# Optimization experiments

Hardware: AMD Instinct MI355X
Metric: run time of the kernel (lower is better)

## Reference

```python
import jax, jax.numpy as jnp
import numpy as np

FLOW_NUM = 2048
H = 64  # lstm_output_dim
NOISE_DIM = 3


def _w(key, shape, s=0.08):
    return (jax.random.normal(key, shape, dtype=jnp.float32) * s)


def setup_inputs() -> dict:
    key = jax.random.key(0)
    ks = jax.random.split(key, 20)
    d = {
        "noise": jax.random.normal(ks[0], (FLOW_NUM, NOISE_DIM), dtype=jnp.float32),
        "w_ih0": _w(ks[1], (4 * H, NOISE_DIM)),
        "w_hh0": _w(ks[2], (4 * H, H)),
        "b_ih0": _w(ks[3], (4 * H,)),
        "b_hh0": _w(ks[4], (4 * H,)),
        "w_ih1": _w(ks[5], (4 * H, H)),
        "w_hh1": _w(ks[6], (4 * H, H)),
        "b_ih1": _w(ks[7], (4 * H,)),
        "b_hh1": _w(ks[8], (4 * H,)),
        "w_ih2": _w(ks[9], (4 * H, H)),
        "w_hh2": _w(ks[10], (4 * H, H)),
        "b_ih2": _w(ks[11], (4 * H,)),
        "b_hh2": _w(ks[12], (4 * H,)),
        "fc1_w": _w(ks[13], (32, H)),
        "fc1_b": _w(ks[14], (32,)),
        "fc2_w": _w(ks[15], (16, 32)),
        "fc2_b": _w(ks[16], (16,)),
        "fc3_w": _w(ks[17], (3, 16)),
        "fc3_b": _w(ks[18], (3,)),
        "flow_length": 500,
    }
    return d


def _lstm_cell(x, h, c, w_ih, w_hh, b_ih, b_hh):
    # PyTorch gate order: input, forget, cell(g), output
    gates = x @ w_ih.T + h @ w_hh.T + (b_ih + b_hh)
    i, f, g, o = jnp.split(gates, 4, axis=-1)
    c_new = jax.nn.sigmoid(f) * c + jax.nn.sigmoid(i) * jnp.tanh(g)
    h_new = jax.nn.sigmoid(o) * jnp.tanh(c_new)
    return h_new, c_new


def reference(noise, w_ih0, w_hh0, b_ih0, b_hh0,
              w_ih1, w_hh1, b_ih1, b_hh1,
              w_ih2, w_hh2, b_ih2, b_hh2,
              fc1_w, fc1_b, fc2_w, fc2_b, fc3_w, fc3_b,
              flow_length):
    layers = [(w_ih0, w_hh0, b_ih0, b_hh0),
              (w_ih1, w_hh1, b_ih1, b_hh1),
              (w_ih2, w_hh2, b_ih2, b_hh2)]
    n = noise.shape[0]
    h0 = jnp.zeros((3, n, H), dtype=noise.dtype)
    c0 = jnp.zeros((3, n, H), dtype=noise.dtype)

    def step(carry, _):
        x, h, c = carry
        inp = x
        hs, cs = [], []
        for l, (wi, wh, bi, bh) in enumerate(layers):
            h_l, c_l = _lstm_cell(inp, h[l], c[l], wi, wh, bi, bh)
            hs.append(h_l)
            cs.append(c_l)
            inp = h_l
        # MLP head (Dropout is identity in eval mode); LeakyReLU slope 0.01
        y = jax.nn.leaky_relu(inp @ fc1_w.T + fc1_b)
        y = jax.nn.leaky_relu(y @ fc2_w.T + fc2_b)
        y = jax.nn.leaky_relu(y @ fc3_w.T + fc3_b)
        return (y, jnp.stack(hs), jnp.stack(cs)), y

    _, flow = jax.lax.scan(step, (noise, h0, c0), None, length=flow_length)
    # flow: [flow_length, flow_num, 3] -> [flow_num, flow_length, 3]
    return jnp.swapaxes(flow, 0, 1)
```

## Files before the change

### kernel.cpp

```cpp
#include <hip/hip_runtime.h>

#define NT 512

typedef _Float16 f16x8 __attribute__((ext_vector_type(8)));
typedef _Float16 f16x4 __attribute__((ext_vector_type(4)));
typedef float    f32x4 __attribute__((ext_vector_type(4)));

#define MFMA(a, b, c) __builtin_amdgcn_mfma_f32_16x16x32_f16((a), (b), (c), 0, 0, 0)

#if __has_builtin(__builtin_amdgcn_exp2f)
__device__ __forceinline__ float fexp(float x) { return __builtin_amdgcn_exp2f(x * 1.4426950408889634f); }
#else
__device__ __forceinline__ float fexp(float x) { return __expf(x); }
#endif
#if __has_builtin(__builtin_amdgcn_rcpf)
__device__ __forceinline__ float frcp(float x) { return __builtin_amdgcn_rcpf(x); }
#else
__device__ __forceinline__ float frcp(float x) { return 1.0f / x; }
#endif
__device__ __forceinline__ float sigm(float x)  { return frcp(1.0f + fexp(-x)); }
__device__ __forceinline__ float tanh_(float x) { return 1.0f - 2.0f * frcp(1.0f + fexp(2.0f * x)); }
__device__ __forceinline__ float lrelu(float x) { return x > 0.0f ? x : 0.01f * x; }

__device__ __forceinline__ f16x8 ld8(const float* p) {
    const float4* q = (const float4*)p;
    float4 a = q[0], b = q[1];
    f16x8 r = { (_Float16)a.x, (_Float16)a.y, (_Float16)a.z, (_Float16)a.w,
                (_Float16)b.x, (_Float16)b.y, (_Float16)b.z, (_Float16)b.w };
    return r;
}

__global__ __launch_bounds__(NT, 2)
void gen_kernel(
    const float* __restrict__ noise,
    const float* __restrict__ w_ih0, const float* __restrict__ w_hh0,
    const float* __restrict__ b_ih0, const float* __restrict__ b_hh0,
    const float* __restrict__ w_ih1, const float* __restrict__ w_hh1,
    const float* __restrict__ b_ih1, const float* __restrict__ b_hh1,
    const float* __restrict__ w_ih2, const float* __restrict__ w_hh2,
    const float* __restrict__ b_ih2, const float* __restrict__ b_hh2,
    const float* __restrict__ fc1_w, const float* __restrict__ fc1_b,
    const float* __restrict__ fc2_w, const float* __restrict__ fc2_b,
    const float* __restrict__ fc3_w, const float* __restrict__ fc3_b,
    const int*   __restrict__ flow_len_p,
    float* __restrict__ out)
{
    __shared__ _Float16 sh[3][2][16 * 64] __attribute__((aligned(16)));
    __shared__ _Float16 sx [16][40] __attribute__((aligned(16)));
    __shared__ _Float16 sy1[16][40] __attribute__((aligned(16)));
    __shared__ _Float16 sy2[16][40] __attribute__((aligned(16)));

    const int tid  = threadIdx.x;
    const int l    = tid & 63;
    const int w    = tid >> 6;
    const int ls   = l & 15;
    const int lj   = l >> 4;
    const int base = blockIdx.x * 8;
    const int T    = flow_len_p[0];

    const int gA  = ls & 3;
    const int rA0 = gA * 64 + 4 * (2 * w + 0) + (ls >> 2);
    const int rA1 = gA * 64 + 4 * (2 * w + 1) + (ls >> 2);

    f16x8 A1[2][4], A2[2][4], A0[2][3];
#pragma unroll
    for (int kc = 0; kc < 2; ++kc) {
        A1[0][kc]     = ld8(w_ih1 + rA0 * 64 + 32 * kc + 8 * lj);
        A1[1][kc]     = ld8(w_ih1 + rA1 * 64 + 32 * kc + 8 * lj);
        A1[0][2 + kc] = ld8(w_hh1 + rA0 * 64 + 32 * kc + 8 * lj);
        A1[1][2 + kc] = ld8(w_hh1 + rA1 * 64 + 32 * kc + 8 * lj);
        A2[0][kc]     = ld8(w_ih2 + rA0 * 64 + 32 * kc + 8 * lj);
        A2[1][kc]     = ld8(w_ih2 + rA1 * 64 + 32 * kc + 8 * lj);
        A2[0][2 + kc] = ld8(w_hh2 + rA0 * 64 + 32 * kc + 8 * lj);
        A2[1][2 + kc] = ld8(w_hh2 + rA1 * 64 + 32 * kc + 8 * lj);
        A0[0][kc]     = ld8(w_hh0 + rA0 * 64 + 32 * kc + 8 * lj);
        A0[1][kc]     = ld8(w_hh0 + rA1 * 64 + 32 * kc + 8 * lj);
    }
#pragma unroll
    for (int tt = 0; tt < 2; ++tt) {
        const int r = tt ? rA1 : rA0;
        f16x8 v;
#pragma unroll
        for (int i = 0; i < 8; ++i) {
            int kl = 8 * lj + i;
            float x = (kl < 3) ? w_ih0[r * 3 + kl]
                    : (kl == 3) ? (b_ih0[r] + b_hh0[r]) : 0.0f;
            v[i] = (_Float16)x;
        }
        A0[tt][2] = v;
    }
    f16x8 F1[2][2], F2, F3;
#pragma unroll
    for (int tt = 0; tt < 2; ++tt)
#pragma unroll
        for (int kc = 0; kc < 2; ++kc)
            F1[tt][kc] = ld8(fc1_w + (16 * tt + ls) * 64 + 32 * kc + 8 * lj);
    F2 = ld8(fc2_w + ls * 32 + 8 * lj);
    {
        f16x8 v;
#pragma unroll
        for (int i = 0; i < 8; ++i) {
            int k = 8 * lj + i;
            v[i] = (_Float16)((ls < 3 && k < 16) ? fc3_w[ls * 16 + k] : 0.0f);
        }
        F3 = v;
    }
    const int uc0 = 8 * w + lj, uc1 = 8 * w + 4 + lj;
    const int u_own = (ls < 8) ? uc0 : uc1;
    const int cs    = ls & 7;
    const int whaddr = cs * 64 + 8 * (((u_own >> 3) + cs) & 7) + (u_own & 7);
    float b1o[4], b2o[4];
#pragma unroll
    for (int g = 0; g < 4; ++g) {
        b1o[g] = b_ih1[g * 64 + u_own] + b_hh1[g * 64 + u_own];
        b2o[g] = b_ih2[g * 64 + u_own] + b_hh2[g * 64 + u_own];
    }
    float hb1a[4], hb1b[4], hb2[4];
#pragma unroll
    for (int r = 0; r < 4; ++r) {
        hb1a[r] = fc1_b[4 * lj + r];
        hb1b[r] = fc1_b[16 + 4 * lj + r];
        hb2[r]  = fc2_b[4 * lj + r];
    }
    float fb3[3] = { fc3_b[0], fc3_b[1], fc3_b[2] };

    for (int i = tid; i < 3 * 2 * 16 * 64; i += NT) ((_Float16*)sh)[i] = (_Float16)0.0f;
    for (int i = tid; i < 16 * 40; i += NT) {
        ((_Float16*)sx)[i]  = (_Float16)0.0f;
        ((_Float16*)sy1)[i] = (_Float16)0.0f;
        ((_Float16*)sy2)[i] = (_Float16)0.0f;
    }
    __syncthreads();
    if (tid < 16) sx[tid][3] = (_Float16)1.0f;
    if (tid < 24) {
        int s = tid / 3, d = tid % 3;
        sx[s][d] = (_Float16)noise[(base + s) * 3 + d];
    }

    float c0s = 0.0f, c1s = 0.0f, c2s = 0.0f;
    const float zb[4] = {0, 0, 0, 0};
    __syncthreads();

#define RD(L, p, kg) (*(const f16x8*)&sh[L][p][ls * 64 + 8 * (((kg) + ls) & 7)])

#define REPACK(cell, a0, a1)                                                   \
    float cell[4];                                                             \
    _Pragma("unroll")                                                          \
    for (int r = 0; r < 4; ++r) {                                              \
        float v_ = __shfl_xor(a1[r], 8);                                       \
        cell[r] = (ls < 8) ? a0[r] : v_;                                       \
    }

#define ACTC(cell, bo, cref, L, p) {                                           \
        float gi = cell[0] + bo[0], gf = cell[1] + bo[1];                      \
        float gg = cell[2] + bo[2], go = cell[3] + bo[3];                      \
        cref = sigm(gf) * cref + sigm(gi) * tanh_(gg);                         \
        sh[L][p][whaddr] = (_Float16)(sigm(go) * tanh_(cref)); }

    {
        f16x8 bx = *(const f16x8*)&sx[ls][8 * lj];
        f32x4 a0 = {0, 0, 0, 0}, a1 = {0, 0, 0, 0};
        a0 = MFMA(A0[0][2], bx, a0);
        a1 = MFMA(A0[1][2], bx, a1);
        REPACK(cell, a0, a1)
        ACTC(cell, zb, c0s, 0, 0)
    }
    __syncthreads();
    f16x8 ph1a = RD(1, 1, lj), ph1b = RD(1, 1, 4 + lj);

    for (int t = 0; t < T; ++t) {
        const int pc = t & 1, pp = pc ^ 1;
        f16x8 r0 = RD(0, pc, lj), r1 = RD(0, pc, 4 + lj);
        f16x8 nh2a = RD(2, pp, lj), nh2b = RD(2, pp, 4 + lj);
        {
            f32x4 a0 = {0, 0, 0, 0}, a1 = {0, 0, 0, 0};
            a0 = MFMA(A1[0][0], r0, a0);   a1 = MFMA(A1[1][0], r0, a1);
            a0 = MFMA(A1[0][1], r1, a0);   a1 = MFMA(A1[1][1], r1, a1);
            a0 = MFMA(A1[0][2], ph1a, a0); a1 = MFMA(A1[1][2], ph1a, a1);
            a0 = MFMA(A1[0][3], ph1b, a0); a1 = MFMA(A1[1][3], ph1b, a1);
            REPACK(cell, a0, a1)
            ACTC(cell, b1o, c1s, 1, pc)
        }
        __syncthreads();
        {
            f16x8 s0 = RD(1, pc, lj), s1 = RD(1, pc, 4 + lj);
            f32x4 a0 = {0, 0, 0, 0}, a1 = {0, 0, 0, 0};
            a0 = MFMA(A2[0][0], s0, a0);   a1 = MFMA(A2[1][0], s0, a1);
            a0 = MFMA(A2[0][1], s1, a0);   a1 = MFMA(A2[1][1], s1, a1);
            a0 = MFMA(A2[0][2], nh2a, a0); a1 = MFMA(A2[1][2], nh2a, a1);
            a0 = MFMA(A2[0][3], nh2b, a0); a1 = MFMA(A2[1][3], nh2b, a1);
            REPACK(cell, a0, a1)
            ACTC(cell, b2o, c2s, 2, pc)
        }
        __syncthreads();
        f32x4 h0a = {0, 0, 0, 0}, h0b = {0, 0, 0, 0};
        h0a = MFMA(A0[0][0], r0, h0a); h0b = MFMA(A0[1][0], r0, h0b);
        h0a = MFMA(A0[0][1], r1, h0a); h0b = MFMA(A0[1][1], r1, h0b);
        if (w == 0) {
            f16x8 bh0 = RD(2, pc, lj), bh1 = RD(2, pc, 4 + lj);
            f32x4 y1a = {0, 0, 0, 0}, y1b = {0, 0, 0, 0};
            y1a = MFMA(F1[0][0], bh0, y1a); y1b = MFMA(F1[1][0], bh0, y1b);
            y1a = MFMA(F1[0][1], bh1, y1a); y1b = MFMA(F1[1][1], bh1, y1b);
            f16x4 v;
#pragma unroll
            for (int r = 0; r < 4; ++r) v[r] = (_Float16)lrelu(y1a[r] + hb1a[r]);
            *(f16x4*)&sy1[ls][4 * lj] = v;
#pragma unroll
            for (int r = 0; r < 4; ++r) v[r] = (_Float16)lrelu(y1b[r] + hb1b[r]);
            *(f16x4*)&sy1[ls][16 + 4 * lj] = v;
            f16x8 by1 = *(const f16x8*)&sy1[ls][8 * lj];
            f32x4 y2 = {0, 0, 0, 0};
            y2 = MFMA(F2, by1, y2);
#pragma unroll
            for (int r = 0; r < 4; ++r) v[r] = (_Float16)lrelu(y2[r] + hb2[r]);
            *(f16x4*)&sy2[ls][4 * lj] = v;
            f16x8 by2 = *(const f16x8*)&sy2[ls][8 * lj];
            f32x4 y3 = {0, 0, 0, 0};
            y3 = MFMA(F3, by2, y3);
            if (lj == 0) {
                float o0 = lrelu(y3[0] + fb3[0]);
                float o1 = lrelu(y3[1] + fb3[1]);
                float o2 = lrelu(y3[2] + fb3[2]);
                sx[ls][0] = (_Float16)o0;
                sx[ls][1] = (_Float16)o1;
                sx[ls][2] = (_Float16)o2;
                if (ls < 8) {
                    float* op = out + ((size_t)(base + ls) * T + t) * 3;
                    op[0] = o0; op[1] = o1; op[2] = o2;
                }
            }
        }
        __syncthreads();
        {
            f16x8 bx = *(const f16x8*)&sx[ls][8 * lj];
            h0a = MFMA(A0[0][2], bx, h0a);
            h0b = MFMA(A0[1][2], bx, h0b);
            REPACK(cell, h0a, h0b)
            ACTC(cell, zb, c0s, 0, pp)
        }
        ph1a = RD(1, pc, lj); ph1b = RD(1, pc, 4 + lj);
        __syncthreads();
    }
}

extern "C" void kernel_launch(void* const* d_in, const int* in_sizes, int n_in,
                              void* d_out, int out_size, void* d_ws, size_t ws_size,
                              hipStream_t stream) {
    const float* noise = (const float*)d_in[0];
    const float* w_ih0 = (const float*)d_in[1];
    const float* w_hh0 = (const float*)d_in[2];
    const float* b_ih0 = (const float*)d_in[3];
    const float* b_hh0 = (const float*)d_in[4];
    const float* w_ih1 = (const float*)d_in[5];
    const float* w_hh1 = (const float*)d_in[6];
    const float* b_ih1 = (const float*)d_in[7];
    const float* b_hh1 = (const float*)d_in[8];
    const float* w_ih2 = (const float*)d_in[9];
    const float* w_hh2 = (const float*)d_in[10];
    const float* b_ih2 = (const float*)d_in[11];
    const float* b_hh2 = (const float*)d_in[12];
    const float* fc1w  = (const float*)d_in[13];
    const float* fc1b  = (const float*)d_in[14];
    const float* fc2w  = (const float*)d_in[15];
    const float* fc2b  = (const float*)d_in[16];
    const float* fc3w  = (const float*)d_in[17];
    const float* fc3b  = (const float*)d_in[18];
    const int*   flp   = (const int*)d_in[19];

    gen_kernel<<<dim3(256), dim3(NT), 0, stream>>>(
        noise, w_ih0, w_hh0, b_ih0, b_hh0,
        w_ih1, w_hh1, b_ih1, b_hh1,
        w_ih2, w_hh2, b_ih2, b_hh2,
        fc1w, fc1b, fc2w, fc2b, fc3w, fc3b,
        flp, (float*)d_out);
}
```

Baseline: 806.7 us.

## Replicate MLP head per wave and keep hidden states in registers to drop barriers

Every wave now computes the MLP head redundantly in its own shared scratch slice. The fc3 output is fed straight from registers into the layer-0 input MFMA, which removes the shared sx buffer and one __syncthreads per timestep. The double-buffered hidden-state arrays become single buffers, with h1/h2 operands carried in registers across iterations. Recurrent and input MFMA chains are split into two independent accumulators to add ILP. The cost is duplicated MLP work across all eight waves and more register pressure.

```diff
diff --git a/kernel.cpp b/kernel.cpp
--- a/kernel.cpp
+++ b/kernel.cpp
@@ -28,6 +28,13 @@
     f16x8 r = { (_Float16)a.x, (_Float16)a.y, (_Float16)a.z, (_Float16)a.w,
                 (_Float16)b.x, (_Float16)b.y, (_Float16)b.z, (_Float16)b.w };
     return r;
+}
+
+__device__ __forceinline__ f16x8 zero8() {
+    f16x8 z;
+#pragma unroll
+    for (int i = 0; i < 8; ++i) z[i] = (_Float16)0.0f;
+    return z;
 }
 
 __global__ __launch_bounds__(NT, 2)
@@ -45,10 +52,9 @@
     const int*   __restrict__ flow_len_p,
     float* __restrict__ out)
 {
-    __shared__ _Float16 sh[3][2][16 * 64] __attribute__((aligned(16)));
-    __shared__ _Float16 sx [16][40] __attribute__((aligned(16)));
-    __shared__ _Float16 sy1[16][40] __attribute__((aligned(16)));
-    __shared__ _Float16 sy2[16][40] __attribute__((aligned(16)));
+    __shared__ _Float16 sh[3][16 * 64] __attribute__((aligned(16)));
+    __shared__ _Float16 sy1[8][16][40] __attribute__((aligned(16)));
+    __shared__ _Float16 sy2[8][16][40] __attribute__((aligned(16)));
 
     const int tid  = threadIdx.x;
     const int l    = tid & 63;
@@ -124,24 +130,17 @@
     }
     float fb3[3] = { fc3_b[0], fc3_b[1], fc3_b[2] };
 
-    for (int i = tid; i < 3 * 2 * 16 * 64; i += NT) ((_Float16*)sh)[i] = (_Float16)0.0f;
-    for (int i = tid; i < 16 * 40; i += NT) {
-        ((_Float16*)sx)[i]  = (_Float16)0.0f;
+    for (int i = tid; i < 3 * 16 * 64; i += NT) ((_Float16*)sh)[i] = (_Float16)0.0f;
+    for (int i = tid; i < 8 * 16 * 40; i += NT) {
         ((_Float16*)sy1)[i] = (_Float16)0.0f;
         ((_Float16*)sy2)[i] = (_Float16)0.0f;
     }
     __syncthreads();
-    if (tid < 16) sx[tid][3] = (_Float16)1.0f;
-    if (tid < 24) {
-        int s = tid / 3, d = tid % 3;
-        sx[s][d] = (_Float16)noise[(base + s) * 3 + d];
-    }
 
     float c0s = 0.0f, c1s = 0.0f, c2s = 0.0f;
     const float zb[4] = {0, 0, 0, 0};
-    __syncthreads();
-
-#define RD(L, p, kg) (*(const f16x8*)&sh[L][p][ls * 64 + 8 * (((kg) + ls) & 7)])
+
+#define RD(L, kg) (*(const f16x8*)&sh[L][ls * 64 + 8 * (((kg) + ls) & 7)])
 
 #define REPACK(cell, a0, a1)                                                   \
     float cell[4];                                                             \
@@ -151,94 +150,99 @@
         cell[r] = (ls < 8) ? a0[r] : v_;                                       \
     }
 
-#define ACTC(cell, bo, cref, L, p) {                                           \
+#define ACTC(cell, bo, cref, L) {                                              \
         float gi = cell[0] + bo[0], gf = cell[1] + bo[1];                      \
         float gg = cell[2] + bo[2], go = cell[3] + bo[3];                      \
         cref = sigm(gf) * cref + sigm(gi) * tanh_(gg);                         \
-        sh[L][p][whaddr] = (_Float16)(sigm(go) * tanh_(cref)); }
+        sh[L][whaddr] = (_Float16)(sigm(go) * tanh_(cref)); }
 
     {
-        f16x8 bx = *(const f16x8*)&sx[ls][8 * lj];
+        f16x8 bx0 = zero8();
+        if (lj == 0) {
+            float n0 = 0.0f, n1 = 0.0f, n2 = 0.0f;
+            if (ls < 8) {
+                const float* np = noise + (size_t)(base + ls) * 3;
+                n0 = np[0]; n1 = np[1]; n2 = np[2];
+            }
+            bx0[0] = (_Float16)n0; bx0[1] = (_Float16)n1;
+            bx0[2] = (_Float16)n2; bx0[3] = (_Float16)1.0f;
+        }
         f32x4 a0 = {0, 0, 0, 0}, a1 = {0, 0, 0, 0};
-        a0 = MFMA(A0[0][2], bx, a0);
-        a1 = MFMA(A0[1][2], bx, a1);
+        a0 = MFMA(A0[0][2], bx0, a0);
+        a1 = MFMA(A0[1][2], bx0, a1);
         REPACK(cell, a0, a1)
-        ACTC(cell, zb, c0s, 0, 0)
-    }
+        ACTC(cell, zb, c0s, 0)
+    }
+    f16x8 h1r0 = zero8(), h1r1 = zero8();
+    f16x8 h2r0 = zero8(), h2r1 = zero8();
     __syncthreads();
-    f16x8 ph1a = RD(1, 1, lj), ph1b = RD(1, 1, 4 + lj);
 
     for (int t = 0; t < T; ++t) {
-        const int pc = t & 1, pp = pc ^ 1;
-        f16x8 r0 = RD(0, pc, lj), r1 = RD(0, pc, 4 + lj);
-        f16x8 nh2a = RD(2, pp, lj), nh2b = RD(2, pp, 4 + lj);
+        f16x8 r0 = RD(0, lj), r1 = RD(0, 4 + lj);
         {
-            f32x4 a0 = {0, 0, 0, 0}, a1 = {0, 0, 0, 0};
-            a0 = MFMA(A1[0][0], r0, a0);   a1 = MFMA(A1[1][0], r0, a1);
-            a0 = MFMA(A1[0][1], r1, a0);   a1 = MFMA(A1[1][1], r1, a1);
-            a0 = MFMA(A1[0][2], ph1a, a0); a1 = MFMA(A1[1][2], ph1a, a1);
-            a0 = MFMA(A1[0][3], ph1b, a0); a1 = MFMA(A1[1][3], ph1b, a1);
+            f32x4 u0 = {0,0,0,0}, u1 = {0,0,0,0}, v0 = {0,0,0,0}, v1 = {0,0,0,0};
+            v0 = MFMA(A1[0][2], h1r0, v0); v1 = MFMA(A1[1][2], h1r0, v1);
+            v0 = MFMA(A1[0][3], h1r1, v0); v1 = MFMA(A1[1][3], h1r1, v1);
+            u0 = MFMA(A1[0][0], r0, u0);   u1 = MFMA(A1[1][0], r0, u1);
+            u0 = MFMA(A1[0][1], r1, u0);   u1 = MFMA(A1[1][1], r1, u1);
+            f32x4 a0 = u0 + v0, a1 = u1 + v1;
             REPACK(cell, a0, a1)
-            ACTC(cell, b1o, c1s, 1, pc)
+            ACTC(cell, b1o, c1s, 1)
         }
         __syncthreads();
+        h1r0 = RD(1, lj); h1r1 = RD(1, 4 + lj);
         {
-            f16x8 s0 = RD(1, pc, lj), s1 = RD(1, pc, 4 + lj);
-            f32x4 a0 = {0, 0, 0, 0}, a1 = {0, 0, 0, 0};
-            a0 = MFMA(A2[0][0], s0, a0);   a1 = MFMA(A2[1][0], s0, a1);
-            a0 = MFMA(A2[0][1], s1, a0);   a1 = MFMA(A2[1][1], s1, a1);
-            a0 = MFMA(A2[0][2], nh2a, a0); a1 = MFMA(A2[1][2], nh2a, a1);
-            a0 = MFMA(A2[0][3], nh2b, a0); a1 = MFMA(A2[1][3], nh2b, a1);
+            f32x4 u0 = {0,0,0,0}, u1 = {0,0,0,0}, v0 = {0,0,0,0}, v1 = {0,0,0,0};
+            v0 = MFMA(A2[0][2], h2r0, v0); v1 = MFMA(A2[1][2], h2r0, v1);
+            v0 = MFMA(A2[0][3], h2r1, v0); v1 = MFMA(A2[1][3], h2r1, v1);
+            u0 = MFMA(A2[0][0], h1r0, u0); u1 = MFMA(A2[1][0], h1r0, u1);
+            u0 = MFMA(A2[0][1], h1r1, u0); u1 = MFMA(A2[1][1], h1r1, u1);
+            f32x4 a0 = u0 + v0, a1 = u1 + v1;
             REPACK(cell, a0, a1)
-            ACTC(cell, b2o, c2s, 2, pc)
+            ACTC(cell, b2o, c2s, 2)
         }
         __syncthreads();
-        f32x4 h0a = {0, 0, 0, 0}, h0b = {0, 0, 0, 0};
-        h0a = MFMA(A0[0][0], r0, h0a); h0b = MFMA(A0[1][0], r0, h0b);
-        h0a = MFMA(A0[0][1], r1, h0a); h0b = MFMA(A0[1][1], r1, h0b);
-        if (w == 0) {
-            f16x8 bh0 = RD(2, pc, lj), bh1 = RD(2, pc, 4 + lj);
-            f32x4 y1a = {0, 0, 0, 0}, y1b = {0, 0, 0, 0};
-            y1a = MFMA(F1[0][0], bh0, y1a); y1b = MFMA(F1[1][0], bh0, y1b);
-            y1a = MFMA(F1[0][1], bh1, y1a); y1b = MFMA(F1[1][1], bh1, y1b);
-            f16x4 v;
-#pragma unroll
-            for (int r = 0; r < 4; ++r) v[r] = (_Float16)lrelu(y1a[r] + hb1a[r]);
-            *(f16x4*)&sy1[ls][4 * lj] = v;
-#pragma unroll
-            for (int r = 0; r < 4; ++r) v[r] = (_Float16)lrelu(y1b[r] + hb1b[r]);
-            *(f16x4*)&sy1[ls][16 + 4 * lj] = v;
-            f16x8 by1 = *(const f16x8*)&sy1[ls][8 * lj];
-            f32x4 y2 = {0, 0, 0, 0};
+        h2r0 = RD(2, lj); h2r1 = RD(2, 4 + lj);
+        {
+            f32x4 h0a = {0,0,0,0}, h0b = {0,0,0,0};
+            h0a = MFMA(A0[0][0], r0, h0a); h0b = MFMA(A0[1][0], r0, h0b);
+            h0a = MFMA(A0[0][1], r1, h0a); h0b = MFMA(A0[1][1], r1, h0b);
+            f32x4 y1a = {0,0,0,0}, y1b = {0,0,0,0};
+            y1a = MFMA(F1[0][0], h2r0, y1a); y1b = MFMA(F1[1][0], h2r0, y1b);
+            y1a = MFMA(F1[0][1], h2r1, y1a); y1b = MFMA(F1[1][1], h2r1, y1b);
+            f16x4 vv;
+#pragma unroll
+            for (int r = 0; r < 4; ++r) vv[r] = (_Float16)lrelu(y1a[r] + hb1a[r]);
+            *(f16x4*)&sy1[w][ls][4 * lj] = vv;
+#pragma unroll
+            for (int r = 0; r < 4; ++r) vv[r] = (_Float16)lrelu(y1b[r] + hb1b[r]);
+            *(f16x4*)&sy1[w][ls][16 + 4 * lj] = vv;
+            f16x8 by1 = *(const f16x8*)&sy1[w][ls][8 * lj];
+            f32x4 y2 = {0,0,0,0};
             y2 = MFMA(F2, by1, y2);
 #pragma unroll
-            for (int r = 0; r < 4; ++r) v[r] = (_Float16)lrelu(y2[r] + hb2[r]);
-            *(f16x4*)&sy2[ls][4 * lj] = v;
-            f16x8 by2 = *(const f16x8*)&sy2[ls][8 * lj];
-            f32x4 y3 = {0, 0, 0, 0};
+            for (int r = 0; r < 4; ++r) vv[r] = (_Float16)lrelu(y2[r] + hb2[r]);
+            *(f16x4*)&sy2[w][ls][4 * lj] = vv;
+            f16x8 by2 = *(const f16x8*)&sy2[w][ls][8 * lj];
+            f32x4 y3 = {0,0,0,0};
             y3 = MFMA(F3, by2, y3);
+            f16x8 bx = zero8();
             if (lj == 0) {
                 float o0 = lrelu(y3[0] + fb3[0]);
                 float o1 = lrelu(y3[1] + fb3[1]);
                 float o2 = lrelu(y3[2] + fb3[2]);
-                sx[ls][0] = (_Float16)o0;
-                sx[ls][1] = (_Float16)o1;
-                sx[ls][2] = (_Float16)o2;
-                if (ls < 8) {
+                bx[0] = (_Float16)o0; bx[1] = (_Float16)o1;
+                bx[2] = (_Float16)o2; bx[3] = (_Float16)1.0f;
+                if (w == 0 && ls < 8) {
                     float* op = out + ((size_t)(base + ls) * T + t) * 3;
                     op[0] = o0; op[1] = o1; op[2] = o2;
                 }
             }
-        }
-        __syncthreads();
-        {
-            f16x8 bx = *(const f16x8*)&sx[ls][8 * lj];
             h0a = MFMA(A0[0][2], bx, h0a);
             h0b = MFMA(A0[1][2], bx, h0b);
             REPACK(cell, h0a, h0b)
-            ACTC(cell, zb, c0s, 0, pp)
-        }
-        ph1a = RD(1, pc, lj); ph1b = RD(1, pc, 4 + lj);
+            ACTC(cell, zb, c0s, 0)
+        }
         __syncthreads();
     }
 }
```

Result: slower. 831.7 us (+3.1%).
